# Kernel tuning notes

Hardware: AMD Instinct MI355X
Metric: run time of the kernel (lower is better)

## Reference

```python
import jax, jax.numpy as jnp
import numpy as np

N = 50000
E = 600000
F_IN = 128
F_OUT = 128


def setup_inputs() -> dict:
    key = jax.random.key(0)
    k = jax.random.split(key, 8)
    x = jax.random.normal(k[0], (N, F_IN), dtype=jnp.float32)
    edge_index = jax.random.randint(k[1], (2, E), 0, N, dtype=jnp.int64)
    edge_weight = jax.random.uniform(k[2], (E,), dtype=jnp.float32)
    # glorot-initialized linear params (w1 is dead code in the original, kept for faithfulness)
    s = float(np.sqrt(6.0 / (F_IN + F_OUT)))
    W1 = jax.random.uniform(k[3], (F_IN, F_OUT), minval=-s, maxval=s, dtype=jnp.float32)
    b1 = jnp.zeros((F_OUT,), dtype=jnp.float32)
    W2 = jax.random.uniform(k[4], (F_IN, F_OUT), minval=-s, maxval=s, dtype=jnp.float32)
    b2 = jnp.zeros((F_OUT,), dtype=jnp.float32)
    a = jnp.full((1,), 0.5, dtype=jnp.float32)
    b = jnp.full((1,), 0.5, dtype=jnp.float32)
    return {"x": x, "edge_index": edge_index, "edge_weight": edge_weight,
            "W1": W1, "b1": b1, "W2": W2, "b2": b2, "a": a, "b": b}


def reference(x, edge_index, edge_weight, W1, b1, W2, b2, a, b):
    # wh_1 = self.w1(x)  (computed but unused in the original forward)
    wh_1 = x @ W1 + b1  # noqa: F841 (dead, DCE'd under jit)
    src, dst = edge_index[0], edge_index[1]
    # gather neighbor features [E, F_IN], scatter-sum to destination nodes [N, F_IN]
    x_j = jax.ops.segment_sum(x[src], dst, num_segments=N)
    wh_2 = x_j @ W2 + b2
    return wh_2
```

## Files before the change

kernel.cpp:

```cpp
#include <hip/hip_runtime.h>

#define F 128
#define CAP 64
#define LDT 136
#define TR 64
#define KC 32
#define LDA 36
#define LDW 160

typedef __attribute__((ext_vector_type(8))) short bf16x8;
typedef __attribute__((ext_vector_type(4))) float f32x4;

__device__ __forceinline__ unsigned short bf16r(float f)
{
    unsigned u = __float_as_uint(f);
    return (unsigned short)((u + 0x7fffu + ((u >> 16) & 1u)) >> 16);
}

__global__ __launch_bounds__(256) void zero_kernel(
    const int* __restrict__ ei, int* __restrict__ flag,
    int* __restrict__ cursor, int N)
{
    int i = blockIdx.x * 256 + threadIdx.x;
    if (i < N) cursor[i] = 0;
    if (i == 0) {
        int or_hi = ei[1] | ei[3] | ei[5] | ei[7] | ei[9] | ei[11] | ei[13] | ei[15];
        *flag = (or_hi == 0) ? 1 : 0;
    }
}

__device__ __forceinline__ void load_edge(const int* __restrict__ ei, int is64,
                                          int E, int e, int& s, int& d)
{
    if (is64) {
        s = reinterpret_cast<const int2*>(ei)[e].x;
        d = reinterpret_cast<const int2*>(ei)[(size_t)E + e].x;
    } else {
        s = ei[e];
        d = ei[E + e];
    }
}

__global__ __launch_bounds__(256) void posconv_kernel(
    const int* __restrict__ ei, const float* __restrict__ x,
    const float* __restrict__ W, const int* __restrict__ flag_p,
    int* __restrict__ cursor, int* __restrict__ csr_src,
    unsigned int* __restrict__ xh, unsigned short* __restrict__ Wt,
    int E, int M)
{
    const int tid = blockIdx.x * 256 + threadIdx.x;
    const int T = gridDim.x * 256;
    const int is64 = *flag_p;

    if (tid < E) {
        int s, d;
        load_edge(ei, is64, E, tid, s, d);
        int slot = atomicAdd(&cursor[d], 1);
        if (slot < CAP) csr_src[d * CAP + slot] = s;
    }

    const float2* x2 = reinterpret_cast<const float2*>(x);
    for (int j = tid; j < M; j += T) {
        float2 v = x2[j];
        xh[j] = (unsigned)bf16r(v.x) | ((unsigned)bf16r(v.y) << 16);
    }

    for (int j = tid; j < F * F; j += T) {
        int k = j >> 7, n = j & 127;
        Wt[n * F + k] = bf16r(W[j]);
    }
}

__device__ __forceinline__ float4 bf16x4_to_f4(uint2 u)
{
    float4 f;
    f.x = __uint_as_float(u.x << 16);
    f.y = __uint_as_float(u.x & 0xffff0000u);
    f.z = __uint_as_float(u.y << 16);
    f.w = __uint_as_float(u.y & 0xffff0000u);
    return f;
}

__global__ __launch_bounds__(256) void gather_bucket_kernel(
    const unsigned int* __restrict__ xh, const int* __restrict__ ei,
    const int* __restrict__ flag_p, const int* __restrict__ cursor,
    const int* __restrict__ csr_src, unsigned int* __restrict__ aggbf,
    int N, int E)
{
    int node = blockIdx.x * 4 + (threadIdx.x >> 6);
    if (node >= N) return;
    int lane = threadIdx.x & 63;
    int half = lane >> 5;
    int col = lane & 31;
    int deg = cursor[node];

    const uint2* x2 = reinterpret_cast<const uint2*>(xh);
    float4 a0 = make_float4(0.f, 0.f, 0.f, 0.f);
    float4 a1 = make_float4(0.f, 0.f, 0.f, 0.f);

    if (deg <= CAP) {
        int sv = (lane < deg) ? csr_src[node * CAP + lane] : 0;
        int i = 0;
        for (; i + 3 < deg; i += 4) {
            int e0 = __shfl(sv, i + half);
            int e1 = __shfl(sv, i + 2 + half);
            float4 v0 = bf16x4_to_f4(x2[(size_t)e0 * 32 + col]);
            float4 v1 = bf16x4_to_f4(x2[(size_t)e1 * 32 + col]);
            a0.x += v0.x; a0.y += v0.y; a0.z += v0.z; a0.w += v0.w;
            a1.x += v1.x; a1.y += v1.y; a1.z += v1.z; a1.w += v1.w;
        }
        for (; i + 1 < deg; i += 2) {
            int e0 = __shfl(sv, i + half);
            float4 v0 = bf16x4_to_f4(x2[(size_t)e0 * 32 + col]);
            a0.x += v0.x; a0.y += v0.y; a0.z += v0.z; a0.w += v0.w;
        }
        if (i < deg) {
            int e0 = __shfl(sv, i);
            if (half == 0) {
                float4 v = bf16x4_to_f4(x2[(size_t)e0 * 32 + col]);
                a0.x += v.x; a0.y += v.y; a0.z += v.z; a0.w += v.w;
            }
        }
    } else {
        int is64 = *flag_p;
        for (int base = 0; base < E; base += 64) {
            int e = base + lane;
            int s = 0, d = -1;
            if (e < E) load_edge(ei, is64, E, e, s, d);
            unsigned long long m = __ballot(d == node);
            while (m) {
                int i = __ffsll((long long)m) - 1;
                m &= m - 1;
                int sb = __shfl(s, i);
                float4 v = bf16x4_to_f4(x2[(size_t)sb * 32 + col]);
                if (half == 0) { a0.x += v.x; a0.y += v.y; a0.z += v.z; a0.w += v.w; }
            }
        }
    }
    a0.x += a1.x; a0.y += a1.y; a0.z += a1.z; a0.w += a1.w;
    a0.x += __shfl_xor(a0.x, 32);
    a0.y += __shfl_xor(a0.y, 32);
    a0.z += __shfl_xor(a0.z, 32);
    a0.w += __shfl_xor(a0.w, 32);
    if (half == 0) {
        uint2 o;
        o.x = (unsigned)bf16r(a0.x) | ((unsigned)bf16r(a0.y) << 16);
        o.y = (unsigned)bf16r(a0.z) | ((unsigned)bf16r(a0.w) << 16);
        reinterpret_cast<uint2*>(aggbf)[(size_t)node * 32 + col] = o;
    }
}

__global__ __launch_bounds__(256) void gemm_mfma_kernel(
    const unsigned short* __restrict__ aggbf, const unsigned short* __restrict__ Wt,
    const float* __restrict__ bias, float* __restrict__ out, int N)
{
    __shared__ unsigned short sWt[F * LDT];
    const int t = threadIdx.x;

    const uint4* Wg = reinterpret_cast<const uint4*>(Wt);
    #pragma unroll
    for (int u = 0; u < 8; ++u) {
        int idx = u * 256 + t;
        int n = idx >> 4;
        int c = idx & 15;
        *reinterpret_cast<uint4*>(&sWt[n * LDT + c * 8]) = Wg[idx];
    }
    __syncthreads();

    const int wv = t >> 6, lane = t & 63;
    const int quad = lane >> 4, n15 = lane & 15;
    const int rbase = blockIdx.x * 64 + wv * 16;

    f32x4 acc[8];
    #pragma unroll
    for (int i = 0; i < 8; ++i) acc[i] = (f32x4){0.f, 0.f, 0.f, 0.f};

    const int arow = rbase + n15;
    const bool aval = (arow < N);
    #pragma unroll
    for (int kc = 0; kc < F; kc += 32) {
        bf16x8 af;
        if (aval)
            af = *reinterpret_cast<const bf16x8*>(aggbf + (size_t)arow * F + kc + quad * 8);
        else
            af = (bf16x8){0, 0, 0, 0, 0, 0, 0, 0};
        #pragma unroll
        for (int nt = 0; nt < 8; ++nt) {
            bf16x8 bfr = *reinterpret_cast<const bf16x8*>(
                &sWt[(nt * 16 + n15) * LDT + kc + quad * 8]);
            acc[nt] = __builtin_amdgcn_mfma_f32_16x16x32_bf16(af, bfr, acc[nt], 0, 0, 0);
        }
    }

    #pragma unroll
    for (int nt = 0; nt < 8; ++nt) {
        float bv = bias[nt * 16 + n15];
        #pragma unroll
        for (int reg = 0; reg < 4; ++reg) {
            int row = rbase + quad * 4 + reg;
            if (row < N)
                out[(size_t)row * F + nt * 16 + n15] = acc[nt][reg] + bv;
        }
    }
}

__global__ __launch_bounds__(256) void init_kernel(
    const int* __restrict__ ei, int* __restrict__ flag,
    int* __restrict__ zero_arr, int N)
{
    int i = blockIdx.x * 256 + threadIdx.x;
    if (i < N) zero_arr[i] = 0;
    if (i == 0) {
        int or_hi = ei[1] | ei[3] | ei[5] | ei[7] | ei[9] | ei[11] | ei[13] | ei[15];
        *flag = (or_hi == 0) ? 1 : 0;
    }
}

__global__ __launch_bounds__(256) void position_bucket_kernel(
    const int* __restrict__ ei, const int* __restrict__ flag_p,
    int* __restrict__ cursor, int* __restrict__ csr_src, int E)
{
    int e = blockIdx.x * 256 + threadIdx.x;
    if (e >= E) return;
    int s, d;
    load_edge(ei, *flag_p, E, e, s, d);
    int slot = atomicAdd(&cursor[d], 1);
    if (slot < CAP) csr_src[d * CAP + slot] = s;
}

__global__ __launch_bounds__(256) void gather_bucket_f32_kernel(
    const float* __restrict__ x, const int* __restrict__ ei,
    const int* __restrict__ flag_p, const int* __restrict__ cursor,
    const int* __restrict__ csr_src, float* __restrict__ agg, int N, int E)
{
    int node = blockIdx.x * 4 + (threadIdx.x >> 6);
    if (node >= N) return;
    int lane = threadIdx.x & 63;
    int half = lane >> 5;
    int col = lane & 31;
    int deg = cursor[node];

    const float4* x4 = reinterpret_cast<const float4*>(x);
    float4 a0 = make_float4(0.f, 0.f, 0.f, 0.f);
    float4 a1 = make_float4(0.f, 0.f, 0.f, 0.f);

    if (deg <= CAP) {
        int sv = (lane < deg) ? csr_src[node * CAP + lane] : 0;
        int i = 0;
        for (; i + 3 < deg; i += 4) {
            int e0 = __shfl(sv, i + half);
            int e1 = __shfl(sv, i + 2 + half);
            float4 v0 = x4[(size_t)e0 * 32 + col];
            float4 v1 = x4[(size_t)e1 * 32 + col];
            a0.x += v0.x; a0.y += v0.y; a0.z += v0.z; a0.w += v0.w;
            a1.x += v1.x; a1.y += v1.y; a1.z += v1.z; a1.w += v1.w;
        }
        for (; i + 1 < deg; i += 2) {
            int e0 = __shfl(sv, i + half);
            float4 v0 = x4[(size_t)e0 * 32 + col];
            a0.x += v0.x; a0.y += v0.y; a0.z += v0.z; a0.w += v0.w;
        }
        if (i < deg) {
            int e0 = __shfl(sv, i);
            if (half == 0) {
                float4 v = x4[(size_t)e0 * 32 + col];
                a0.x += v.x; a0.y += v.y; a0.z += v.z; a0.w += v.w;
            }
        }
    } else {
        int is64 = *flag_p;
        for (int base = 0; base < E; base += 64) {
            int e = base + lane;
            int s = 0, d = -1;
            if (e < E) load_edge(ei, is64, E, e, s, d);
            unsigned long long m = __ballot(d == node);
            while (m) {
                int i = __ffsll((long long)m) - 1;
                m &= m - 1;
                int sb = __shfl(s, i);
                float4 v = x4[(size_t)sb * 32 + col];
                if (half == 0) { a0.x += v.x; a0.y += v.y; a0.z += v.z; a0.w += v.w; }
            }
        }
    }
    a0.x += a1.x; a0.y += a1.y; a0.z += a1.z; a0.w += a1.w;
    a0.x += __shfl_xor(a0.x, 32);
    a0.y += __shfl_xor(a0.y, 32);
    a0.z += __shfl_xor(a0.z, 32);
    a0.w += __shfl_xor(a0.w, 32);
    if (half == 0)
        reinterpret_cast<float4*>(agg)[(size_t)node * 32 + col] = a0;
}

__global__ __launch_bounds__(256) void scatter_kernel(
    const float* __restrict__ x, const int* __restrict__ ei,
    const int* __restrict__ flag_p, float* __restrict__ agg, int E)
{
    int tid = blockIdx.x * 256 + threadIdx.x;
    int e = tid >> 5;
    if (e >= E) return;
    int c = (tid & 31) << 2;
    int s, d;
    load_edge(ei, *flag_p, E, e, s, d);
    float4 v = *reinterpret_cast<const float4*>(x + (size_t)s * F + c);
    float* o = agg + (size_t)d * F + c;
    unsafeAtomicAdd(o + 0, v.x);
    unsafeAtomicAdd(o + 1, v.y);
    unsafeAtomicAdd(o + 2, v.z);
    unsafeAtomicAdd(o + 3, v.w);
}

__global__ __launch_bounds__(256) void gemm_kernel(
    float* __restrict__ io, const float* __restrict__ W,
    const float* __restrict__ bias, int N)
{
    __shared__ float sA[TR * LDA];
    __shared__ float sW[KC * LDW];
    const int t = threadIdx.x;
    const int row0 = blockIdx.x * TR;
    const int g = t & 7;
    const int r = t >> 3;

    float acc[2][16];
    #pragma unroll
    for (int i = 0; i < 2; ++i)
        #pragma unroll
        for (int j = 0; j < 16; ++j) acc[i][j] = 0.0f;

    for (int kc = 0; kc < F; kc += KC) {
        #pragma unroll
        for (int u = 0; u < 2; ++u) {
            int idx = u * 256 + t;
            int row = idx >> 3;
            int k4 = (idx & 7) * 4;
            int grow = row0 + row;
            float4 v = (grow < N)
                ? *reinterpret_cast<const float4*>(io + (size_t)grow * F + kc + k4)
                : make_float4(0.f, 0.f, 0.f, 0.f);
            *reinterpret_cast<float4*>(&sA[row * LDA + k4]) = v;
        }
        #pragma unroll
        for (int u = 0; u < 4; ++u) {
            int idx = u * 256 + t;
            int kk = idx >> 5;
            int f4 = (idx & 31) * 4;
            float4 v = *reinterpret_cast<const float4*>(W + (size_t)(kc + kk) * F + f4);
            int chunk = f4 >> 4;
            int within = f4 & 15;
            *reinterpret_cast<float4*>(&sW[kk * LDW + chunk * 20 + within]) = v;
        }
        __syncthreads();

        #pragma unroll 8
        for (int kk = 0; kk < KC; ++kk) {
            const float* wp = &sW[kk * LDW + g * 20];
            const float4 w0 = *reinterpret_cast<const float4*>(wp + 0);
            const float4 w1 = *reinterpret_cast<const float4*>(wp + 4);
            const float4 w2 = *reinterpret_cast<const float4*>(wp + 8);
            const float4 w3 = *reinterpret_cast<const float4*>(wp + 12);
            #pragma unroll
            for (int i = 0; i < 2; ++i) {
                const float xv = sA[(r * 2 + i) * LDA + kk];
                acc[i][0]  += xv * w0.x;  acc[i][1]  += xv * w0.y;
                acc[i][2]  += xv * w0.z;  acc[i][3]  += xv * w0.w;
                acc[i][4]  += xv * w1.x;  acc[i][5]  += xv * w1.y;
                acc[i][6]  += xv * w1.z;  acc[i][7]  += xv * w1.w;
                acc[i][8]  += xv * w2.x;  acc[i][9]  += xv * w2.y;
                acc[i][10] += xv * w2.z;  acc[i][11] += xv * w2.w;
                acc[i][12] += xv * w3.x;  acc[i][13] += xv * w3.y;
                acc[i][14] += xv * w3.z;  acc[i][15] += xv * w3.w;
            }
        }
        __syncthreads();
    }

    float bv[16];
    #pragma unroll
    for (int j = 0; j < 16; ++j) bv[j] = bias[g * 16 + j];
    #pragma unroll
    for (int i = 0; i < 2; ++i) {
        int row = row0 + r * 2 + i;
        if (row < N) {
            float* o = io + (size_t)row * F + g * 16;
            #pragma unroll
            for (int j4 = 0; j4 < 4; ++j4) {
                float4 v;
                v.x = acc[i][j4 * 4 + 0] + bv[j4 * 4 + 0];
                v.y = acc[i][j4 * 4 + 1] + bv[j4 * 4 + 1];
                v.z = acc[i][j4 * 4 + 2] + bv[j4 * 4 + 2];
                v.w = acc[i][j4 * 4 + 3] + bv[j4 * 4 + 3];
                *reinterpret_cast<float4*>(o + j4 * 4) = v;
            }
        }
    }
}

extern "C" void kernel_launch(void* const* d_in, const int* in_sizes, int n_in,
                              void* d_out, int out_size, void* d_ws, size_t ws_size,
                              hipStream_t stream) {
    const float* x  = (const float*)d_in[0];
    const int*   ei = (const int*)d_in[1];
    const float* W2 = (const float*)d_in[5];
    const float* b2 = (const float*)d_in[6];
    float* out = (float*)d_out;

    const int N = in_sizes[0] / F;
    const int E = in_sizes[2];
    const int nblk = (N + 255) / 256;
    const int M = N * (F / 2);
    const int eblk = (E + 255) / 256;

    int* ws = (int*)d_ws;
    size_t needA = (size_t)(16 + N + (size_t)N * CAP + M + (F * F / 2) + (size_t)N * (F / 2))
                   * sizeof(int);
    size_t needB = (size_t)(16 + N + (size_t)N * CAP) * sizeof(int);

    if (ws_size >= needA) {
        int* flag    = ws;
        int* cursor  = flag + 16;
        int* csr_src = cursor + N;
        unsigned int*   xh    = (unsigned int*)(csr_src + (size_t)N * CAP);
        unsigned short* Wt    = (unsigned short*)(xh + M);
        unsigned int*   aggbf = (unsigned int*)(Wt + F * F);

        zero_kernel<<<nblk, 256, 0, stream>>>(ei, flag, cursor, N);
        posconv_kernel<<<eblk, 256, 0, stream>>>(ei, x, W2, flag, cursor, csr_src,
                                                 xh, Wt, E, M);
        gather_bucket_kernel<<<(N + 3) / 4, 256, 0, stream>>>(
            xh, ei, flag, cursor, csr_src, aggbf, N, E);
        gemm_mfma_kernel<<<(N + 63) / 64, 256, 0, stream>>>(
            (const unsigned short*)aggbf, Wt, b2, out, N);
    } else if (ws_size >= needB) {
        int* flag    = ws;
        int* cursor  = flag + 16;
        int* csr_src = cursor + N;
        init_kernel<<<nblk, 256, 0, stream>>>(ei, flag, cursor, N);
        position_bucket_kernel<<<eblk, 256, 0, stream>>>(ei, flag, cursor, csr_src, E);
        gather_bucket_f32_kernel<<<(N + 3) / 4, 256, 0, stream>>>(
            x, ei, flag, cursor, csr_src, out, N, E);
        gemm_kernel<<<(N + TR - 1) / TR, 256, 0, stream>>>(out, W2, b2, N);
    } else {
        int* flag = ws;
        init_kernel<<<1, 64, 0, stream>>>(ei, flag, flag + 16, 0);
        hipMemsetAsync(out, 0, (size_t)N * F * sizeof(float), stream);
        scatter_kernel<<<(E * 32 + 255) / 256, 256, 0, stream>>>(x, ei, flag, out, E);
        gemm_kernel<<<(N + TR - 1) / TR, 256, 0, stream>>>(out, W2, b2, N);
    }
}
```

Measured before the change: 165.9 us.

## Restructure prep: fuse zero+convert, 4-edge bucketing, 16-bit CSR indices

Merges the cursor zeroing, flag detection, x-to-bf16 conversion and W transpose into one prep kernel. Edge bucketing moves into its own kernel where each thread vectorizes loads of four edges. Source indices are stored as 16-bit values, halving CSR bucket traffic in both the bucketing and gather stages. The 16-bit path is restricted to N <= 65536 and falls back to the older paths otherwise. The bucketing launch still depends on prep finishing first, so the two stages stay serialized.

```diff
diff --git a/kernel.cpp b/kernel.cpp
--- a/kernel.cpp
+++ b/kernel.cpp
@@ -17,18 +17,6 @@
     return (unsigned short)((u + 0x7fffu + ((u >> 16) & 1u)) >> 16);
 }
 
-__global__ __launch_bounds__(256) void zero_kernel(
-    const int* __restrict__ ei, int* __restrict__ flag,
-    int* __restrict__ cursor, int N)
-{
-    int i = blockIdx.x * 256 + threadIdx.x;
-    if (i < N) cursor[i] = 0;
-    if (i == 0) {
-        int or_hi = ei[1] | ei[3] | ei[5] | ei[7] | ei[9] | ei[11] | ei[13] | ei[15];
-        *flag = (or_hi == 0) ? 1 : 0;
-    }
-}
-
 __device__ __forceinline__ void load_edge(const int* __restrict__ ei, int is64,
                                           int E, int e, int& s, int& d)
 {
@@ -41,34 +29,67 @@
     }
 }
 
-__global__ __launch_bounds__(256) void posconv_kernel(
+__global__ __launch_bounds__(256) void prep_kernel(
     const int* __restrict__ ei, const float* __restrict__ x,
-    const float* __restrict__ W, const int* __restrict__ flag_p,
-    int* __restrict__ cursor, int* __restrict__ csr_src,
-    unsigned int* __restrict__ xh, unsigned short* __restrict__ Wt,
-    int E, int M)
+    const float* __restrict__ W, int* __restrict__ flag,
+    int* __restrict__ cursor, unsigned int* __restrict__ xh,
+    unsigned short* __restrict__ Wt, int N, int M)
+{
+    int i = blockIdx.x * 256 + threadIdx.x;
+    if (i < M) {
+        float2 v = reinterpret_cast<const float2*>(x)[i];
+        xh[i] = (unsigned)bf16r(v.x) | ((unsigned)bf16r(v.y) << 16);
+    }
+    if (i < N) cursor[i] = 0;
+    if (i < F * F) {
+        int k = i >> 7, n = i & 127;
+        Wt[n * F + k] = bf16r(W[i]);
+    }
+    if (i == 0) {
+        int or_hi = ei[1] | ei[3] | ei[5] | ei[7] | ei[9] | ei[11] | ei[13] | ei[15];
+        *flag = (or_hi == 0) ? 1 : 0;
+    }
+}
+
+__global__ __launch_bounds__(256) void position4_kernel(
+    const int* __restrict__ ei, const int* __restrict__ flag_p,
+    int* __restrict__ cursor, unsigned short* __restrict__ csr16, int E)
 {
     const int tid = blockIdx.x * 256 + threadIdx.x;
-    const int T = gridDim.x * 256;
+    const int base = 4 * tid;
+    if (base >= E) return;
     const int is64 = *flag_p;
 
-    if (tid < E) {
-        int s, d;
-        load_edge(ei, is64, E, tid, s, d);
-        int slot = atomicAdd(&cursor[d], 1);
-        if (slot < CAP) csr_src[d * CAP + slot] = s;
-    }
-
-    const float2* x2 = reinterpret_cast<const float2*>(x);
-    for (int j = tid; j < M; j += T) {
-        float2 v = x2[j];
-        xh[j] = (unsigned)bf16r(v.x) | ((unsigned)bf16r(v.y) << 16);
-    }
-
-    for (int j = tid; j < F * F; j += T) {
-        int k = j >> 7, n = j & 127;
-        Wt[n * F + k] = bf16r(W[j]);
-    }
+    int s[4], d[4];
+    int cnt;
+    if (base + 3 < E && (E & 3) == 0) {
+        cnt = 4;
+        if (is64) {
+            const int4* sp = reinterpret_cast<const int4*>(ei);
+            int4 a = sp[tid * 2], b = sp[tid * 2 + 1];
+            s[0] = a.x; s[1] = a.z; s[2] = b.x; s[3] = b.z;
+            const int4* dp = reinterpret_cast<const int4*>(ei) + ((size_t)E >> 1);
+            int4 c = dp[tid * 2], e4 = dp[tid * 2 + 1];
+            d[0] = c.x; d[1] = c.z; d[2] = e4.x; d[3] = e4.z;
+        } else {
+            int4 sv = reinterpret_cast<const int4*>(ei)[tid];
+            int4 dv = reinterpret_cast<const int4*>(ei + E)[tid];
+            s[0] = sv.x; s[1] = sv.y; s[2] = sv.z; s[3] = sv.w;
+            d[0] = dv.x; d[1] = dv.y; d[2] = dv.z; d[3] = dv.w;
+        }
+    } else {
+        cnt = E - base; if (cnt > 4) cnt = 4;
+        for (int j = 0; j < cnt; ++j) load_edge(ei, is64, E, base + j, s[j], d[j]);
+        for (int j = cnt; j < 4; ++j) { s[j] = 0; d[j] = 0; }
+    }
+
+    int slot[4];
+    #pragma unroll
+    for (int j = 0; j < 4; ++j)
+        slot[j] = (j < cnt) ? atomicAdd(&cursor[d[j]], 1) : CAP;
+    #pragma unroll
+    for (int j = 0; j < 4; ++j)
+        if (slot[j] < CAP) csr16[(size_t)d[j] * CAP + slot[j]] = (unsigned short)s[j];
 }
 
 __device__ __forceinline__ float4 bf16x4_to_f4(uint2 u)
@@ -84,7 +105,7 @@
 __global__ __launch_bounds__(256) void gather_bucket_kernel(
     const unsigned int* __restrict__ xh, const int* __restrict__ ei,
     const int* __restrict__ flag_p, const int* __restrict__ cursor,
-    const int* __restrict__ csr_src, unsigned int* __restrict__ aggbf,
+    const unsigned short* __restrict__ csr16, unsigned int* __restrict__ aggbf,
     int N, int E)
 {
     int node = blockIdx.x * 4 + (threadIdx.x >> 6);
@@ -99,7 +120,7 @@
     float4 a1 = make_float4(0.f, 0.f, 0.f, 0.f);
 
     if (deg <= CAP) {
-        int sv = (lane < deg) ? csr_src[node * CAP + lane] : 0;
+        int sv = (lane < deg) ? (int)csr16[(size_t)node * CAP + lane] : 0;
         int i = 0;
         for (; i + 3 < deg; i += 4) {
             int e0 = __shfl(sv, i + half);
@@ -225,7 +246,7 @@
     int s, d;
     load_edge(ei, *flag_p, E, e, s, d);
     int slot = atomicAdd(&cursor[d], 1);
-    if (slot < CAP) csr_src[d * CAP + slot] = s;
+    if (slot < CAP) csr_src[(size_t)d * CAP + slot] = s;
 }
 
 __global__ __launch_bounds__(256) void gather_bucket_f32_kernel(
@@ -245,7 +266,7 @@
     float4 a1 = make_float4(0.f, 0.f, 0.f, 0.f);
 
     if (deg <= CAP) {
-        int sv = (lane < deg) ? csr_src[node * CAP + lane] : 0;
+        int sv = (lane < deg) ? csr_src[(size_t)node * CAP + lane] : 0;
         int i = 0;
         for (; i + 3 < deg; i += 4) {
             int e0 = __shfl(sv, i + half);
@@ -411,23 +432,25 @@
     const int eblk = (E + 255) / 256;
 
     int* ws = (int*)d_ws;
-    size_t needA = (size_t)(16 + N + (size_t)N * CAP + M + (F * F / 2) + (size_t)N * (F / 2))
-                   * sizeof(int);
+    size_t needA = (size_t)16 * 4 + (size_t)N * 4 + (size_t)N * CAP * 2
+                 + (size_t)M * 4 + (size_t)F * F * 2 + (size_t)N * (F / 2) * 4;
     size_t needB = (size_t)(16 + N + (size_t)N * CAP) * sizeof(int);
 
-    if (ws_size >= needA) {
+    if (ws_size >= needA && N <= 65536) {
         int* flag    = ws;
         int* cursor  = flag + 16;
-        int* csr_src = cursor + N;
-        unsigned int*   xh    = (unsigned int*)(csr_src + (size_t)N * CAP);
+        unsigned short* csr16 = (unsigned short*)(cursor + N);
+        unsigned int*   xh    = (unsigned int*)(csr16 + (size_t)N * CAP);
         unsigned short* Wt    = (unsigned short*)(xh + M);
         unsigned int*   aggbf = (unsigned int*)(Wt + F * F);
 
-        zero_kernel<<<nblk, 256, 0, stream>>>(ei, flag, cursor, N);
-        posconv_kernel<<<eblk, 256, 0, stream>>>(ei, x, W2, flag, cursor, csr_src,
-                                                 xh, Wt, E, M);
+        int pmax = M; if (N > pmax) pmax = N; if (F * F > pmax) pmax = F * F;
+        prep_kernel<<<(pmax + 255) / 256, 256, 0, stream>>>(
+            ei, x, W2, flag, cursor, xh, Wt, N, M);
+        int pblk = ((E + 3) / 4 + 255) / 256;
+        position4_kernel<<<pblk, 256, 0, stream>>>(ei, flag, cursor, csr16, E);
         gather_bucket_kernel<<<(N + 3) / 4, 256, 0, stream>>>(
-            xh, ei, flag, cursor, csr_src, aggbf, N, E);
+            xh, ei, flag, cursor, csr16, aggbf, N, E);
         gemm_mfma_kernel<<<(N + 63) / 64, 256, 0, stream>>>(
             (const unsigned short*)aggbf, Wt, b2, out, N);
     } else if (ws_size >= needB) {
```

Measured after the change: 161.4 us. 2.7% less time.
